# Optimization experiments

Measured on AMD Instinct MI355X. Metric: run time of the kernel, lower is better.

## Reference

```python
import jax, jax.numpy as jnp
import numpy as np

TAU = 0.6  # BGK relaxation time (>= 0.5 per __post_init__ stability check)
# D2Q9 lattice: velocities, weights, opposite-direction indices
E = np.array([[0, 0], [1, 0], [0, 1], [-1, 0], [0, -1],
              [1, 1], [-1, 1], [-1, -1], [1, -1]], dtype=np.int32)
W = np.array([4.0 / 9] + [1.0 / 9] * 4 + [1.0 / 36] * 4, dtype=np.float32)
OPP = np.array([0, 3, 4, 1, 2, 7, 8, 5, 6], dtype=np.int32)


def setup_inputs() -> dict:
    key = jax.random.key(0)
    k1, k2, k3 = jax.random.split(key, 3)
    nx, ny = 2048, 2048
    f = jax.random.uniform(k1, (nx, ny, 9), dtype=jnp.float32)  # positive populations
    rho = jnp.sum(f, axis=-1)                                    # consistent density
    u = 0.05 * jax.random.normal(k2, (nx, ny, 2), dtype=jnp.float32)  # low-Ma velocity
    obstacle_mask = jax.random.uniform(k3, (nx, ny)) < 0.01      # sparse solid cells
    return {"f": f, "rho": rho, "u": u, "obstacle_mask": obstacle_mask}


def _equilibrium(rho, u):
    # feq_i = w_i * rho * (1 + 3 e.u + 4.5 (e.u)^2 - 1.5 u.u)
    e = jnp.asarray(E, jnp.float32)
    w = jnp.asarray(W)
    eu = jnp.einsum('xyd,qd->xyq', u, e)              # [nx, ny, 9]
    usq = jnp.sum(u * u, axis=-1, keepdims=True)       # [nx, ny, 1]
    return w * rho[..., None] * (1.0 + 3.0 * eu + 4.5 * eu * eu - 1.5 * usq)


def reference(f, rho, u, obstacle_mask):
    # --- collide (BGK) ---
    feq = _equilibrium(rho, u)
    f_star = f - (f - feq) / TAU
    # --- stream: roll each direction by its lattice velocity (lattice not shifted) ---
    f_new = jnp.stack(
        [jnp.roll(f_star[..., i], shift=(int(E[i, 0]), int(E[i, 1])), axis=(0, 1))
         for i in range(9)],
        axis=-1,
    )
    # --- obstacle bounce-back: solid cells reflect post-collision populations ---
    f_bb = f_star[..., jnp.asarray(OPP)]
    f_new = jnp.where(obstacle_mask[..., None], f_bb, f_new)
    # --- lift macro fields from post-stream distributions ---
    rho_new = jnp.sum(f_new, axis=-1)
    e = jnp.asarray(E, jnp.float32)
    u_new = jnp.einsum('xyq,qd->xyd', f_new, e) / rho_new[..., None]
    # pack (f_new [..9], rho_new [..1], u_new [..2]) -> [nx, ny, 12]
    return jnp.concatenate([f_new, rho_new[..., None], u_new], axis=-1)
```

## Files before the change

### kernel.cpp

```cpp
#include <hip/hip_runtime.h>


#define NX 2048
#define NY 2048
#define WRAP 2047
#define TR 4
#define TC 64
#define HR (TR + 2)
#define HC (TC + 2)
#define HCELLS (HR * HC)
#define HELEMS (HCELLS * 9)

typedef float floatx4 __attribute__((ext_vector_type(4)));

__global__ __launch_bounds__(256) void lbm_step_kernel(
    const float* __restrict__ f,
    const float* __restrict__ rho,
    const float* __restrict__ u,
    const int*   __restrict__ mask,
    float*       __restrict__ out)
{
    __shared__ float lds[HELEMS];

    const int tid = threadIdx.x;
    const int y0 = blockIdx.x * TC;
    const int x0 = blockIdx.y * TR;
    const float INV_TAU = 1.0f / 0.6f;

    const float2* __restrict__ u2 = reinterpret_cast<const float2*>(u);

    for (int k = tid; k < HELEMS; k += 256) {
        const unsigned cell = (unsigned)k / 9u;
        const int i  = k - (int)cell * 9;
        const unsigned hr = cell / (unsigned)HC;
        const int hc = (int)cell - (int)hr * HC;
        const int xr = (x0 - 1 + (int)hr) & WRAP;
        const int yc = (y0 - 1 + hc) & WRAP;
        const int g  = xr * NY + yc;

        const float  rn = rho[g];
        const float2 uv = u2[g];
        const float  fi = f[(size_t)g * 9 + i];

        const float exf = (float)((int)((0x20919u >> (2 * i)) & 3u) - 1);
        const float eyf = (float)((int)((0x2865u  >> (2 * i)) & 3u) - 1);
        const float wi  = (i == 0) ? (4.0f / 9.0f)
                                   : ((i < 5) ? (1.0f / 9.0f) : (1.0f / 36.0f));
        const float eu  = exf * uv.x + eyf * uv.y;
        const float usq = uv.x * uv.x + uv.y * uv.y;
        const float feq = wi * rn * (1.0f + 3.0f * eu + 4.5f * eu * eu - 1.5f * usq);
        lds[k] = fi - (fi - feq) * INV_TAU;
    }
    __syncthreads();

    const int r = tid >> 6;
    const int c = tid & 63;
    const int ex9[9]  = {0, 1, 0, -1, 0, 1, -1, -1, 1};
    const int ey9[9]  = {0, 0, 1, 0, -1, 1, 1, -1, -1};
    const int opp9[9] = {0, 3, 4, 1, 2, 7, 8, 5, 6};

    float fn[9];
    #pragma unroll
    for (int i = 0; i < 9; ++i) {
        const int lsrc = (r + 1 - ex9[i]) * HC + (c + 1 - ey9[i]);
        fn[i] = lds[lsrc * 9 + i];
    }

    const int x = x0 + r, y = y0 + c;
    const int cidx = x * NY + y;
    if (mask[cidx]) {
        const int lc = (r + 1) * HC + (c + 1);
        float fs[9];
        #pragma unroll
        for (int i = 0; i < 9; ++i) fs[i] = lds[lc * 9 + i];
        #pragma unroll
        for (int i = 0; i < 9; ++i) fn[i] = fs[opp9[i]];
    }

    const float rhon = fn[0] + fn[1] + fn[2] + fn[3] + fn[4]
                     + fn[5] + fn[6] + fn[7] + fn[8];
    const float uxn = (fn[1] - fn[3] + fn[5] - fn[6] - fn[7] + fn[8]) / rhon;
    const float uyn = (fn[2] - fn[4] + fn[5] + fn[6] - fn[7] - fn[8]) / rhon;

    __syncthreads();

    {
        const int b = tid * 13;
        #pragma unroll
        for (int i = 0; i < 9; ++i) lds[b + i] = fn[i];
        lds[b + 9]  = rhon;
        lds[b + 10] = uxn;
        lds[b + 11] = uyn;
    }
    __syncthreads();

    for (int k4 = tid; k4 < TR * TC * 3; k4 += 256) {
        const unsigned r2  = (unsigned)k4 / 192u;
        const int      rem = k4 - (int)r2 * 192;
        const unsigned cc  = (unsigned)rem / 3u;
        const int      q   = rem - (int)cc * 3;
        const int lbase = (int)r2 * (TC * 13) + (int)cc * 13 + q * 4;
        floatx4 v;
        v.x = lds[lbase + 0];
        v.y = lds[lbase + 1];
        v.z = lds[lbase + 2];
        v.w = lds[lbase + 3];
        const size_t obase = ((size_t)(x0 + (int)r2) * NY + y0) * 12 + (size_t)rem * 4;
        __builtin_nontemporal_store(v, reinterpret_cast<floatx4*>(out + obase));
    }
}

extern "C" void kernel_launch(void* const* d_in, const int* in_sizes, int n_in,
                              void* d_out, int out_size, void* d_ws, size_t ws_size,
                              hipStream_t stream) {
    const float* f    = (const float*)d_in[0];
    const float* rho  = (const float*)d_in[1];
    const float* u    = (const float*)d_in[2];
    const int*   mask = (const int*)d_in[3];
    float* out = (float*)d_out;

    dim3 block(256, 1, 1);
    dim3 grid(NY / TC, NX / TR, 1);
    lbm_step_kernel<<<grid, block, 0, stream>>>(f, rho, u, mask, out);
}
```

Baseline: 376.7 us.

## Enlarge tile, prefetch populations into registers, precompute per-cell equilibrium terms

Doubles the tile height to 8 rows with 512 threads, which cuts the halo overhead per output cell. All f loads are issued up front into registers. A per-cell cache in LDS holds precomputed rho and u terms, so each population no longer reloads rho and u and redoes the usq math. Division is replaced with the hardware reciprocal and the mask load is hoisted early; this raises register pressure and LDS use and uses slightly less accurate reciprocals.

```diff
diff --git a/kernel.cpp b/kernel.cpp
--- a/kernel.cpp
+++ b/kernel.cpp
@@ -4,23 +4,28 @@
 #define NX 2048
 #define NY 2048
 #define WRAP 2047
-#define TR 4
+#define TR 8
 #define TC 64
+#define NT 512
 #define HR (TR + 2)
 #define HC (TC + 2)
 #define HCELLS (HR * HC)
 #define HELEMS (HCELLS * 9)
+#define CACHEF (HCELLS * 4)
+#define FP_ITERS 12
+#define STAGE_WORDS (NT * 13)
 
 typedef float floatx4 __attribute__((ext_vector_type(4)));
 
-__global__ __launch_bounds__(256) void lbm_step_kernel(
+__global__ __launch_bounds__(NT) void lbm_step_kernel(
     const float* __restrict__ f,
     const float* __restrict__ rho,
     const float* __restrict__ u,
     const int*   __restrict__ mask,
     float*       __restrict__ out)
 {
-    __shared__ float lds[HELEMS];
+    __shared__ float lds[HELEMS + CACHEF];
+    floatx4* cache = reinterpret_cast<floatx4*>(lds + HELEMS);
 
     const int tid = threadIdx.x;
     const int y0 = blockIdx.x * TC;
@@ -29,32 +34,64 @@
 
     const float2* __restrict__ u2 = reinterpret_cast<const float2*>(u);
 
-    for (int k = tid; k < HELEMS; k += 256) {
-        const unsigned cell = (unsigned)k / 9u;
-        const int i  = k - (int)cell * 9;
-        const unsigned hr = cell / (unsigned)HC;
-        const int hc = (int)cell - (int)hr * HC;
+    float fpre[FP_ITERS];
+    #pragma unroll
+    for (int it = 0; it < FP_ITERS; ++it) {
+        const int k = tid + it * NT;
+        if (k < HELEMS) {
+            const unsigned cell = (unsigned)k / 9u;
+            const int i  = k - (int)cell * 9;
+            const unsigned hr = cell / (unsigned)HC;
+            const int hc = (int)cell - (int)hr * HC;
+            const int xr = (x0 - 1 + (int)hr) & WRAP;
+            const int yc = (y0 - 1 + hc) & WRAP;
+            const int g  = xr * NY + yc;
+            fpre[it] = f[(size_t)g * 9 + i];
+        }
+    }
+
+    const int r = tid >> 6;
+    const int c = tid & 63;
+    const int cidx = (x0 + r) * NY + (y0 + c);
+    const int m = mask[cidx];
+
+    for (int k = tid; k < HCELLS; k += NT) {
+        const unsigned hr = (unsigned)k / (unsigned)HC;
+        const int hc = k - (int)hr * HC;
         const int xr = (x0 - 1 + (int)hr) & WRAP;
         const int yc = (y0 - 1 + hc) & WRAP;
         const int g  = xr * NY + yc;
-
         const float  rn = rho[g];
         const float2 uv = u2[g];
-        const float  fi = f[(size_t)g * 9 + i];
-
-        const float exf = (float)((int)((0x20919u >> (2 * i)) & 3u) - 1);
-        const float eyf = (float)((int)((0x2865u  >> (2 * i)) & 3u) - 1);
-        const float wi  = (i == 0) ? (4.0f / 9.0f)
-                                   : ((i < 5) ? (1.0f / 9.0f) : (1.0f / 36.0f));
-        const float eu  = exf * uv.x + eyf * uv.y;
         const float usq = uv.x * uv.x + uv.y * uv.y;
-        const float feq = wi * rn * (1.0f + 3.0f * eu + 4.5f * eu * eu - 1.5f * usq);
-        lds[k] = fi - (fi - feq) * INV_TAU;
+        floatx4 v;
+        v.x = rn - 1.5f * rn * usq;
+        v.y = 3.0f * rn * uv.x;
+        v.z = 3.0f * rn * uv.y;
+        v.w = __builtin_amdgcn_rcpf(rn + rn);
+        cache[k] = v;
     }
     __syncthreads();
 
-    const int r = tid >> 6;
-    const int c = tid & 63;
+    #pragma unroll
+    for (int it = 0; it < FP_ITERS; ++it) {
+        const int k = tid + it * NT;
+        if (k < HELEMS) {
+            const unsigned cell = (unsigned)k / 9u;
+            const int i  = k - (int)cell * 9;
+            const floatx4 v = cache[cell];
+            const float exf = (float)((int)((0x20919u >> (2 * i)) & 3u) - 1);
+            const float eyf = (float)((int)((0x2865u  >> (2 * i)) & 3u) - 1);
+            const float wi  = (i == 0) ? (4.0f / 9.0f)
+                                       : ((i < 5) ? (1.0f / 9.0f) : (1.0f / 36.0f));
+            const float t   = v.y * exf + v.z * eyf;
+            const float feq = wi * (v.x + t + t * t * v.w);
+            const float fi  = fpre[it];
+            lds[k] = fi - (fi - feq) * INV_TAU;
+        }
+    }
+    __syncthreads();
+
     const int ex9[9]  = {0, 1, 0, -1, 0, 1, -1, -1, 1};
     const int ey9[9]  = {0, 0, 1, 0, -1, 1, 1, -1, -1};
     const int opp9[9] = {0, 3, 4, 1, 2, 7, 8, 5, 6};
@@ -65,22 +102,17 @@
         const int lsrc = (r + 1 - ex9[i]) * HC + (c + 1 - ey9[i]);
         fn[i] = lds[lsrc * 9 + i];
     }
-
-    const int x = x0 + r, y = y0 + c;
-    const int cidx = x * NY + y;
-    if (mask[cidx]) {
-        const int lc = (r + 1) * HC + (c + 1);
-        float fs[9];
+    if (m) {
+        const int lc = ((r + 1) * HC + (c + 1)) * 9;
         #pragma unroll
-        for (int i = 0; i < 9; ++i) fs[i] = lds[lc * 9 + i];
-        #pragma unroll
-        for (int i = 0; i < 9; ++i) fn[i] = fs[opp9[i]];
+        for (int i = 0; i < 9; ++i) fn[i] = lds[lc + opp9[i]];
     }
 
     const float rhon = fn[0] + fn[1] + fn[2] + fn[3] + fn[4]
                      + fn[5] + fn[6] + fn[7] + fn[8];
-    const float uxn = (fn[1] - fn[3] + fn[5] - fn[6] - fn[7] + fn[8]) / rhon;
-    const float uyn = (fn[2] - fn[4] + fn[5] + fn[6] - fn[7] - fn[8]) / rhon;
+    const float irho = __builtin_amdgcn_rcpf(rhon);
+    const float uxn = (fn[1] - fn[3] + fn[5] - fn[6] - fn[7] + fn[8]) * irho;
+    const float uyn = (fn[2] - fn[4] + fn[5] + fn[6] - fn[7] - fn[8]) * irho;
 
     __syncthreads();
 
@@ -94,7 +126,9 @@
     }
     __syncthreads();
 
-    for (int k4 = tid; k4 < TR * TC * 3; k4 += 256) {
+    #pragma unroll
+    for (int it = 0; it < 3; ++it) {
+        const int k4 = tid + it * NT;
         const unsigned r2  = (unsigned)k4 / 192u;
         const int      rem = k4 - (int)r2 * 192;
         const unsigned cc  = (unsigned)rem / 3u;
@@ -119,7 +153,7 @@
     const int*   mask = (const int*)d_in[3];
     float* out = (float*)d_out;
 
-    dim3 block(256, 1, 1);
+    dim3 block(NT, 1, 1);
     dim3 grid(NY / TC, NX / TR, 1);
     lbm_step_kernel<<<grid, block, 0, stream>>>(f, rho, u, mask, out);
 }
```

Result: faster. 349.4 us (-7.2%).
